# Kernel optimization log

Hardware: AMD Instinct MI355X
Metric: run time of the kernel (lower is better)

The kernel has to match this reference:

```python
import jax, jax.numpy as jnp
import numpy as np
from jax.scipy.special import logsumexp

T = 2048   # trajectory length
S = 512    # state dim (self.s)
B = 16     # number of options (self.b)
A = 18     # number of actions (self.a)
PEN = 0.5  # abstract_penalty
NEG = -1e9 # padding log-prob for not-yet-created option rows


def setup_inputs() -> dict:
    key = jax.random.key(0)
    k1, k2, k3, k4, k5 = jax.random.split(key, 5)
    s_i = jax.random.normal(k1, (T + 1, S), dtype=jnp.float32)
    W_action = jax.random.normal(k2, (S, B * A), dtype=jnp.float32) * 0.05
    W_stop = jax.random.normal(k3, (S, B * 2), dtype=jnp.float32) * 0.05
    W_start = jax.random.normal(k4, (S, B), dtype=jnp.float32) * 0.05
    actions = jax.random.randint(k5, (T,), 0, A, dtype=jnp.int64)
    return {"s_i": s_i, "W_action": W_action, "W_stop": W_stop,
            "W_start": W_start, "actions": actions}


def _hmm_logp(s_i, W_action, W_stop, W_start, actions):
    # abstract_policy_net: linear heads + log_softmax over the relevant axis
    action_logps = jax.nn.log_softmax((s_i @ W_action).reshape(T + 1, B, A), axis=-1)
    stop_logps = jax.nn.log_softmax((s_i @ W_stop).reshape(T + 1, B, 2), axis=-1)
    start_logps = jax.nn.log_softmax(s_i @ W_start, axis=-1)  # (T+1, B)

    # padded option_step_dist buffer: row i is created at step i (torch.cat append)
    buf0 = jnp.full((T, B), NEG, dtype=s_i.dtype).at[0].set(start_logps[0])

    def step(carry, xs):
        buf, tot = carry
        i, act = xs
        stop = stop_logps[i]          # (B, 2)
        start_lps = start_logps[i]    # (B,)
        # rearrange mass: options that stop get redistributed to new starts
        total_rearrange = logsumexp(buf + stop[:, 1]) - PEN
        new_mass = start_lps + total_rearrange
        buf2 = (buf + stop[:, 0]).at[i].set(new_mass)
        buf = jnp.where(i > 0, buf2, buf)  # i == 0 skips the rearrange branch
        action_lps = action_logps[i, :, act]  # (B,)
        tot = tot + logsumexp(action_lps + buf)
        return (buf, tot), None

    xs = (jnp.arange(T), actions)
    (buf, total_logp), _ = jax.lax.scan(step, (buf0, jnp.asarray(0.0, s_i.dtype)), xs)
    # final: all options must stop (note original uses index 0 here, as in source)
    total_logp = total_logp + logsumexp(stop_logps[-1, :, 0] + buf)
    return total_logp


def reference(s_i, W_action, W_stop, W_start, actions):
    return _hmm_logp(s_i, W_action, W_stop, W_start, actions)
```

## Files before the change

kernel.cpp:

```cpp
#include <hip/hip_runtime.h>

#define TT    2048
#define SS    512
#define NB    16
#define EPEN  0.60653065971263342f
#define NCHUNK 64
#define CLEN   32

typedef __attribute__((ext_vector_type(4))) float  floatx4;
typedef __attribute__((ext_vector_type(8))) short  bf16x8;

__device__ __forceinline__ ushort f2bf(float x) {
  unsigned u = __float_as_uint(x);
  u += 0x7fffu + ((u >> 16) & 1u);
  return (ushort)(u >> 16);
}

__device__ __forceinline__ unsigned pack2(ushort a, ushort b) {
  return (unsigned)a | ((unsigned)b << 16);
}

__global__ __launch_bounds__(256) void prep_kernel(
    const float* __restrict__ Wa, const float* __restrict__ Ws,
    const float* __restrict__ Wst, const float* __restrict__ s_i,
    ushort* __restrict__ Wt2, ushort* __restrict__ Af)
{
  int fid = blockIdx.x * 256 + threadIdx.x;
  if (fid < 21504) {
    const int q = fid & 3, rc = (fid >> 2) & 15, kt = (fid >> 6) & 15, colt = fid >> 10;
    const int col = colt * 16 + rc;
    const int kbase = kt * 32 + q * 8;
    ushort h[8];
    #pragma unroll
    for (int e = 0; e < 8; ++e) {
      const int k = kbase + e;
      float v;
      if (col < 288)      v = Wa [(size_t)k * 288 + col];
      else if (col < 320) v = Ws [(size_t)k * 32  + (col - 288)];
      else                v = Wst[(size_t)k * 16  + (col - 320)];
      h[e] = f2bf(v);
    }
    uint4 o = make_uint4(pack2(h[0], h[1]), pack2(h[2], h[3]),
                         pack2(h[4], h[5]), pack2(h[6], h[7]));
    *(uint4*)(Wt2 + (size_t)fid * 8) = o;
  } else {
    const int aid = fid - 21504;
    if (aid < 132096) {
      const int q = aid & 3, rc = (aid >> 2) & 15, kt = (aid >> 6) & 15, mt = aid >> 10;
      int row = mt * 16 + rc; if (row > TT) row = TT;
      const float* src = s_i + (size_t)row * SS + kt * 32 + q * 8;
      float4 v0 = *(const float4*)src;
      float4 v1 = *(const float4*)(src + 4);
      uint4 o = make_uint4(pack2(f2bf(v0.x), f2bf(v0.y)),
                           pack2(f2bf(v0.z), f2bf(v0.w)),
                           pack2(f2bf(v1.x), f2bf(v1.y)),
                           pack2(f2bf(v1.z), f2bf(v1.w)));
      *(uint4*)(Af + (size_t)aid * 8) = o;
    }
  }
}

__global__ __launch_bounds__(512) void proj_kernel(
    const ushort* __restrict__ Af,
    const ushort* __restrict__ Wt2,
    const int*   __restrict__ actions,
    float4*      __restrict__ coef)
{
  __shared__ float lg[16][346];

  const int tid  = threadIdx.x;
  const int wave = tid >> 6, lane = tid & 63;
  const int q = lane >> 4, rc = lane & 15;
  const int row0 = blockIdx.x * 16;

  const int kh = wave >> 2;
  const int ng = wave & 3;
  const int ntiles = (ng == 0) ? 6 : 5;
  const int kt0 = kh * 8;

  const ushort* aBase = Af  + (size_t)blockIdx.x * 8192 + rc * 32 + q * 8;
  const ushort* bBase = Wt2 + rc * 32 + q * 8;

  floatx4 acc[6];
  #pragma unroll
  for (int j = 0; j < 6; ++j) acc[j] = (floatx4)(0.f);

  bf16x8 aC, aN, bC[6], bN[6];

  aC = *(const bf16x8*)(aBase + kt0 * 512);
  #pragma unroll
  for (int j = 0; j < 6; ++j) {
    if (j < ntiles) {
      const int colt = ng + 4 * j;
      bC[j] = *(const bf16x8*)(bBase + (size_t)colt * 8192 + kt0 * 512);
    }
  }

  #pragma unroll
  for (int kk = 0; kk < 8; ++kk) {
    const int kt = kt0 + kk;
    if (kk < 7) {
      aN = *(const bf16x8*)(aBase + (kt + 1) * 512);
      #pragma unroll
      for (int j = 0; j < 6; ++j) {
        if (j < ntiles) {
          const int colt = ng + 4 * j;
          bN[j] = *(const bf16x8*)(bBase + (size_t)colt * 8192 + (kt + 1) * 512);
        }
      }
    }
    #pragma unroll
    for (int j = 0; j < 6; ++j) {
      if (j < ntiles)
        acc[j] = __builtin_amdgcn_mfma_f32_16x16x32_bf16(aC, bC[j], acc[j], 0, 0, 0);
    }
    aC = aN;
    #pragma unroll
    for (int j = 0; j < 6; ++j) {
      if (j < ntiles) bC[j] = bN[j];
    }
  }

  if (kh == 0) {
    #pragma unroll
    for (int j = 0; j < 6; ++j) {
      if (j < ntiles) {
        const int colt = ng + 4 * j;
        #pragma unroll
        for (int reg = 0; reg < 4; ++reg)
          lg[q * 4 + reg][colt * 16 + rc] = acc[j][reg];
      }
    }
  }
  __syncthreads();
  if (kh == 1) {
    #pragma unroll
    for (int j = 0; j < 6; ++j) {
      if (j < ntiles) {
        const int colt = ng + 4 * j;
        #pragma unroll
        for (int reg = 0; reg < 4; ++reg)
          lg[q * 4 + reg][colt * 16 + rc] += acc[j][reg];
      }
    }
  }
  __syncthreads();

  if (tid < 256) {
    const int r = tid >> 4, b = tid & 15;
    const int row = row0 + r;
    if (row < TT) {
      float m = -3.4e38f;
      #pragma unroll
      for (int a = 0; a < 18; ++a) m = fmaxf(m, lg[r][b * 18 + a]);
      float sum = 0.f;
      #pragma unroll
      for (int a = 0; a < 18; ++a) sum += __expf(lg[r][b * 18 + a] - m);
      int act = actions[row];
      float aprob = __expf(lg[r][b * 18 + act] - m) / sum;

      float x0 = lg[r][288 + 2 * b], x1 = lg[r][288 + 2 * b + 1];
      float mm = fmaxf(x0, x1);
      float e0 = __expf(x0 - mm), e1 = __expf(x1 - mm);
      float inv = 1.f / (e0 + e1);

      float ms = -3.4e38f;
      #pragma unroll
      for (int j = 0; j < 16; ++j) ms = fmaxf(ms, lg[r][320 + j]);
      float ssum = 0.f;
      #pragma unroll
      for (int j = 0; j < 16; ++j) ssum += __expf(lg[r][320 + j] - ms);
      float stp = __expf(lg[r][320 + b] - ms) / ssum;

      coef[(size_t)row * NB + b] = make_float4(e0 * inv, e1 * inv, stp, aprob);
    } else if (row == TT) {
      float x0 = lg[r][288 + 2 * b], x1 = lg[r][288 + 2 * b + 1];
      float mm = fmaxf(x0, x1);
      float e0 = __expf(x0 - mm), e1 = __expf(x1 - mm);
      coef[(size_t)TT * NB + b] = make_float4(1.f, 0.f, 0.f, e0 / (e0 + e1));
    }
  }
}

__global__ __launch_bounds__(64) void pass1_kernel(
    const float4* __restrict__ coef,
    float* __restrict__ Wws, float* __restrict__ Mws)
{
  const int chunk = blockIdx.x * 4 + (threadIdx.x >> 4);
  const int c = threadIdx.x & 15;
  const int i0 = chunk * CLEN + 1;

  float G[16];
  #pragma unroll
  for (int r = 0; r < 16; ++r) G[r] = (r == c) ? 1.f : 0.f;

  float4 cfA[16], cfB[16];
  #pragma unroll
  for (int r = 0; r < 16; ++r) cfA[r] = coef[(size_t)i0 * 16 + r];
  #pragma unroll
  for (int r = 0; r < 16; ++r) cfB[r] = coef[(size_t)(i0 + 1) * 16 + r];

#define P1BODY(CUR, NXT, J)                                                  \
  {                                                                          \
    if ((J) + 2 < CLEN) {                                                    \
      _Pragma("unroll")                                                      \
      for (int r = 0; r < 16; ++r)                                           \
        NXT[r] = coef[(size_t)(i0 + (J) + 2) * 16 + r];                      \
    }                                                                        \
    float ta = 0.f, tb = 0.f, tc = 0.f, td = 0.f;                            \
    _Pragma("unroll")                                                        \
    for (int r = 0; r < 4; ++r) {                                            \
      ta = fmaf(CUR[r].y,      G[r],      ta);                               \
      tb = fmaf(CUR[r + 4].y,  G[r + 4],  tb);                               \
      tc = fmaf(CUR[r + 8].y,  G[r + 8],  tc);                               \
      td = fmaf(CUR[r + 12].y, G[r + 12], td);                               \
    }                                                                        \
    float et = EPEN * ((ta + tb) + (tc + td));                               \
    _Pragma("unroll")                                                        \
    for (int r = 0; r < 16; ++r)                                             \
      G[r] = fmaf(CUR[r].x, G[r], CUR[r].z * et);                            \
    float wa = 0.f, wb = 0.f, wc = 0.f, wd = 0.f;                            \
    _Pragma("unroll")                                                        \
    for (int r = 0; r < 4; ++r) {                                            \
      wa = fmaf(CUR[r].w,      G[r],      wa);                               \
      wb = fmaf(CUR[r + 4].w,  G[r + 4],  wb);                               \
      wc = fmaf(CUR[r + 8].w,  G[r + 8],  wc);                               \
      wd = fmaf(CUR[r + 12].w, G[r + 12], wd);                               \
    }                                                                        \
    Wws[(size_t)(chunk * CLEN + (J)) * 16 + c] = (wa + wb) + (wc + wd);      \
  }

  for (int j = 0; j < CLEN; j += 2) {
    P1BODY(cfA, cfB, j);
    P1BODY(cfB, cfA, j + 1);
  }
#undef P1BODY

  #pragma unroll
  for (int r = 0; r < 16; ++r)
    Mws[chunk * 256 + r * 16 + c] = G[r];
}

__global__ __launch_bounds__(512) void pass2_kernel(
    const float4* __restrict__ coef,
    const float* __restrict__ Wws, const float* __restrict__ Mws,
    float* __restrict__ out)
{
  __shared__ float pbuf[NCHUNK][16];
  __shared__ float wacc[8];

  const int tid = threadIdx.x;
  long long Ktot = 0;

  if (tid < 64) {
    const int r = tid >> 2, g = tid & 3;
    float pj0 = coef[4 * g + 0].z;
    float pj1 = coef[4 * g + 1].z;
    float pj2 = coef[4 * g + 2].z;
    float pj3 = coef[4 * g + 3].z;

    const int moff = r * 16 + 4 * g;
    const int gb0 = 64 * g, gb1 = gb0 + 16, gb2 = gb0 + 32, gb3 = gb0 + 48;
    int Ecum = 0;

    float4 mR0 = *(const float4*)&Mws[0 * 256 + moff];
    float4 mR1 = *(const float4*)&Mws[1 * 256 + moff];
    float4 mR2 = *(const float4*)&Mws[2 * 256 + moff];
    float4 mR3 = *(const float4*)&Mws[3 * 256 + moff];
    float4 mR4 = *(const float4*)&Mws[4 * 256 + moff];
    float4 mR5 = *(const float4*)&Mws[5 * 256 + moff];
    float4 mR6 = *(const float4*)&Mws[6 * 256 + moff];
    float4 mR7 = *(const float4*)&Mws[7 * 256 + moff];

#define P2BODY(K, MREG, KPF)                                                 \
    {                                                                        \
      if (r == 0)                                                            \
        *(float4*)&pbuf[(K)][4 * g] = make_float4(pj0, pj1, pj2, pj3);       \
      Ktot += 32LL * (long long)Ecum;                                        \
      float part = fmaf(MREG.x, pj0,                                         \
                   fmaf(MREG.y, pj1, fmaf(MREG.z, pj2, MREG.w * pj3)));      \
      if ((KPF) < NCHUNK)                                                    \
        MREG = *(const float4*)&Mws[(KPF) * 256 + moff];                     \
              \
      part += __int_as_float(__builtin_amdgcn_mov_dpp(                       \
          __float_as_int(part), 0x39, 0xF, 0xF, true));      \
      part += __int_as_float(__builtin_amdgcn_mov_dpp(                       \
          __float_as_int(part), 0x4E, 0xF, 0xF, true));      \
      int ip = __float_as_int(part);                                         \
      float n0 = __int_as_float(__builtin_amdgcn_ds_bpermute(gb0, ip));      \
      float n1 = __int_as_float(__builtin_amdgcn_ds_bpermute(gb1, ip));      \
      float n2 = __int_as_float(__builtin_amdgcn_ds_bpermute(gb2, ip));      \
      float n3 = __int_as_float(__builtin_amdgcn_ds_bpermute(gb3, ip));      \
      int y0b = __builtin_amdgcn_readfirstlane(__float_as_int(n0));          \
      int eb = (y0b >> 23) & 255;                                            \
      Ecum += eb - 127;                                                      \
      float sc = __int_as_float((254 - eb) << 23);                           \
      pj0 = n0 * sc; pj1 = n1 * sc; pj2 = n2 * sc; pj3 = n3 * sc;            \
    }

    for (int kb = 0; kb < NCHUNK; kb += 8) {
      P2BODY(kb + 0, mR0, kb + 8);
      P2BODY(kb + 1, mR1, kb + 9);
      P2BODY(kb + 2, mR2, kb + 10);
      P2BODY(kb + 3, mR3, kb + 11);
      P2BODY(kb + 4, mR4, kb + 12);
      P2BODY(kb + 5, mR5, kb + 13);
      P2BODY(kb + 6, mR6, kb + 14);
      P2BODY(kb + 7, mR7, kb + 15);
    }
#undef P2BODY
  }
  __syncthreads();

  const int j0 = tid * 4;
  const int chunk = j0 >> 5;
  float p[16];
  #pragma unroll
  for (int c = 0; c < 16; ++c) p[c] = pbuf[chunk][c];

  float lacc = 0.f;
  #pragma unroll
  for (int jj = 0; jj < 4; ++jj) {
    const float* w = Wws + (size_t)(j0 + jj) * 16;
    float4 w0 = *(const float4*)(w);
    float4 w1 = *(const float4*)(w + 4);
    float4 w2 = *(const float4*)(w + 8);
    float4 w3 = *(const float4*)(w + 12);
    float s0 = fmaf(w0.x, p[0],  fmaf(w0.y, p[1],  fmaf(w0.z, p[2],  w0.w * p[3])));
    float s1 = fmaf(w1.x, p[4],  fmaf(w1.y, p[5],  fmaf(w1.z, p[6],  w1.w * p[7])));
    float s2 = fmaf(w2.x, p[8],  fmaf(w2.y, p[9],  fmaf(w2.z, p[10], w2.w * p[11])));
    float s3 = fmaf(w3.x, p[12], fmaf(w3.y, p[13], fmaf(w3.z, p[14], w3.w * p[15])));
    lacc += __logf((s0 + s1) + (s2 + s3));
  }

  if (tid == 0) {
    float U0 = 0.f;
    #pragma unroll
    for (int c = 0; c < 16; ++c) U0 = fmaf(coef[c].w, coef[c].z, U0);
    lacc += __logf(U0);
  }

  lacc += __shfl_xor(lacc, 1, 64);
  lacc += __shfl_xor(lacc, 2, 64);
  lacc += __shfl_xor(lacc, 4, 64);
  lacc += __shfl_xor(lacc, 8, 64);
  lacc += __shfl_xor(lacc, 16, 64);
  lacc += __shfl_xor(lacc, 32, 64);
  if ((tid & 63) == 0) wacc[tid >> 6] = lacc;
  __syncthreads();
  if (tid == 0) {
    double s = 0.0;
    #pragma unroll
    for (int i = 0; i < 8; ++i) s += (double)wacc[i];
    out[0] = (float)(s + 0.6931471805599453 * (double)Ktot);
  }
}

extern "C" void kernel_launch(void* const* d_in, const int* in_sizes, int n_in,
                              void* d_out, int out_size, void* d_ws, size_t ws_size,
                              hipStream_t stream) {
  const float* s_i = (const float*)d_in[0];
  const float* Wa  = (const float*)d_in[1];
  const float* Ws  = (const float*)d_in[2];
  const float* Wst = (const float*)d_in[3];
  const int*   act = (const int*)d_in[4];

  char* ws = (char*)d_ws;
  float4* coef = (float4*)ws;
  float*  Wws  = (float*)(ws + 524544);
  float*  Mws  = (float*)(ws + 524544 + 131072);
  ushort* Wt2  = (ushort*)(ws + 721152);
  ushort* Af   = (ushort*)(ws + 1065216);

  prep_kernel <<<600, 256, 0, stream>>>(Wa, Ws, Wst, s_i, Wt2, Af);
  proj_kernel <<<129, 512, 0, stream>>>(Af, Wt2, act, coef);
  pass1_kernel<<<16,  64,  0, stream>>>(coef, Wws, Mws);
  pass2_kernel<<<1,   512, 0, stream>>>(coef, Wws, Mws, (float*)d_out);
}
```

Before: 98.11 us.

## Fuse s_i bf16 conversion into projection kernel via shared memory tile

Activation conversion from fp32 to bf16 moves out of the prep kernel and into the projection kernel. Each block now converts its own 16-row slice into an LDS tile, so the separate global Af buffer write and reread goes away and the prep launch shrinks to cover only the weights. In pass2, the exponent is read through a ds_bpermute from lane 0 instead of readfirstlane. This adds an LDS round trip and a block-wide sync at the start of the projection kernel.

```diff
diff --git a/kernel.cpp b/kernel.cpp
--- a/kernel.cpp
+++ b/kernel.cpp
@@ -22,50 +22,35 @@
 
 __global__ __launch_bounds__(256) void prep_kernel(
     const float* __restrict__ Wa, const float* __restrict__ Ws,
-    const float* __restrict__ Wst, const float* __restrict__ s_i,
-    ushort* __restrict__ Wt2, ushort* __restrict__ Af)
+    const float* __restrict__ Wst, ushort* __restrict__ Wt2)
 {
   int fid = blockIdx.x * 256 + threadIdx.x;
-  if (fid < 21504) {
-    const int q = fid & 3, rc = (fid >> 2) & 15, kt = (fid >> 6) & 15, colt = fid >> 10;
-    const int col = colt * 16 + rc;
-    const int kbase = kt * 32 + q * 8;
-    ushort h[8];
-    #pragma unroll
-    for (int e = 0; e < 8; ++e) {
-      const int k = kbase + e;
-      float v;
-      if (col < 288)      v = Wa [(size_t)k * 288 + col];
-      else if (col < 320) v = Ws [(size_t)k * 32  + (col - 288)];
-      else                v = Wst[(size_t)k * 16  + (col - 320)];
-      h[e] = f2bf(v);
-    }
-    uint4 o = make_uint4(pack2(h[0], h[1]), pack2(h[2], h[3]),
-                         pack2(h[4], h[5]), pack2(h[6], h[7]));
-    *(uint4*)(Wt2 + (size_t)fid * 8) = o;
-  } else {
-    const int aid = fid - 21504;
-    if (aid < 132096) {
-      const int q = aid & 3, rc = (aid >> 2) & 15, kt = (aid >> 6) & 15, mt = aid >> 10;
-      int row = mt * 16 + rc; if (row > TT) row = TT;
-      const float* src = s_i + (size_t)row * SS + kt * 32 + q * 8;
-      float4 v0 = *(const float4*)src;
-      float4 v1 = *(const float4*)(src + 4);
-      uint4 o = make_uint4(pack2(f2bf(v0.x), f2bf(v0.y)),
-                           pack2(f2bf(v0.z), f2bf(v0.w)),
-                           pack2(f2bf(v1.x), f2bf(v1.y)),
-                           pack2(f2bf(v1.z), f2bf(v1.w)));
-      *(uint4*)(Af + (size_t)aid * 8) = o;
-    }
-  }
+  if (fid >= 21504) return;
+  const int q = fid & 3, rc = (fid >> 2) & 15, kt = (fid >> 6) & 15, colt = fid >> 10;
+  const int col = colt * 16 + rc;
+  const int kbase = kt * 32 + q * 8;
+  ushort h[8];
+  #pragma unroll
+  for (int e = 0; e < 8; ++e) {
+    const int k = kbase + e;
+    float v;
+    if (col < 288)      v = Wa [(size_t)k * 288 + col];
+    else if (col < 320) v = Ws [(size_t)k * 32  + (col - 288)];
+    else                v = Wst[(size_t)k * 16  + (col - 320)];
+    h[e] = f2bf(v);
+  }
+  uint4 o = make_uint4(pack2(h[0], h[1]), pack2(h[2], h[3]),
+                       pack2(h[4], h[5]), pack2(h[6], h[7]));
+  *(uint4*)(Wt2 + (size_t)fid * 8) = o;
 }
 
 __global__ __launch_bounds__(512) void proj_kernel(
-    const ushort* __restrict__ Af,
+    const float* __restrict__ s_i,
     const ushort* __restrict__ Wt2,
     const int*   __restrict__ actions,
     float4*      __restrict__ coef)
 {
+  __shared__ __align__(16) ushort At[8192];
   __shared__ float lg[16][346];
 
   const int tid  = threadIdx.x;
@@ -73,12 +58,28 @@
   const int q = lane >> 4, rc = lane & 15;
   const int row0 = blockIdx.x * 16;
 
+  #pragma unroll
+  for (int u = 0; u < 2; ++u) {
+    const int uid = tid + u * 512;
+    const int qq = uid & 3, rr = (uid >> 2) & 15, kt = uid >> 6;
+    int row = row0 + rr; if (row > TT) row = TT;
+    const float* src = s_i + (size_t)row * SS + kt * 32 + qq * 8;
+    float4 v0 = *(const float4*)src;
+    float4 v1 = *(const float4*)(src + 4);
+    uint4 o = make_uint4(pack2(f2bf(v0.x), f2bf(v0.y)),
+                         pack2(f2bf(v0.z), f2bf(v0.w)),
+                         pack2(f2bf(v1.x), f2bf(v1.y)),
+                         pack2(f2bf(v1.z), f2bf(v1.w)));
+    *(uint4*)(At + (size_t)uid * 8) = o;
+  }
+  __syncthreads();
+
   const int kh = wave >> 2;
   const int ng = wave & 3;
   const int ntiles = (ng == 0) ? 6 : 5;
   const int kt0 = kh * 8;
 
-  const ushort* aBase = Af  + (size_t)blockIdx.x * 8192 + rc * 32 + q * 8;
+  const ushort* aBase = At  + rc * 32 + q * 8;
   const ushort* bBase = Wt2 + rc * 32 + q * 8;
 
   floatx4 acc[6];
@@ -291,8 +292,8 @@
       float n1 = __int_as_float(__builtin_amdgcn_ds_bpermute(gb1, ip));      \
       float n2 = __int_as_float(__builtin_amdgcn_ds_bpermute(gb2, ip));      \
       float n3 = __int_as_float(__builtin_amdgcn_ds_bpermute(gb3, ip));      \
-      int y0b = __builtin_amdgcn_readfirstlane(__float_as_int(n0));          \
-      int eb = (y0b >> 23) & 255;                                            \
+      float y0 = __int_as_float(__builtin_amdgcn_ds_bpermute(0,   ip));      \
+      int eb = (__float_as_int(y0) >> 23) & 255;                             \
       Ecum += eb - 127;                                                      \
       float sc = __int_as_float((254 - eb) << 23);                           \
       pj0 = n0 * sc; pj1 = n1 * sc; pj2 = n2 * sc; pj3 = n3 * sc;            \
@@ -370,10 +371,9 @@
   float*  Wws  = (float*)(ws + 524544);
   float*  Mws  = (float*)(ws + 524544 + 131072);
   ushort* Wt2  = (ushort*)(ws + 721152);
-  ushort* Af   = (ushort*)(ws + 1065216);
-
-  prep_kernel <<<600, 256, 0, stream>>>(Wa, Ws, Wst, s_i, Wt2, Af);
-  proj_kernel <<<129, 512, 0, stream>>>(Af, Wt2, act, coef);
+
+  prep_kernel <<<84,  256, 0, stream>>>(Wa, Ws, Wst, Wt2);
+  proj_kernel <<<129, 512, 0, stream>>>(s_i, Wt2, act, coef);
   pass1_kernel<<<16,  64,  0, stream>>>(coef, Wws, Mws);
   pass2_kernel<<<1,   512, 0, stream>>>(coef, Wws, Mws, (float*)d_out);
 }
```

Measured after the change: 96.88 us. About the same (-1.2%).
